# Kernel tuning notes

Hardware: AMD Instinct MI355X
Metric: run time of the kernel (lower is better)

## Reference

```python
import jax, jax.numpy as jnp
import numpy as np

EPS = 1e-15
MAX_TANH_ARG = 1.0 - 1e-5


def log_map_zero(x, c):
    sqrt_c = c ** 0.5
    n = jnp.clip(jnp.linalg.norm(x, axis=-1, keepdims=True), EPS, None)
    return jnp.arctanh(jnp.clip(sqrt_c * n, None, MAX_TANH_ARG)) * x / (sqrt_c * n)


def exp_map_zero(v, c):
    sqrt_c = c ** 0.5
    n = jnp.clip(jnp.linalg.norm(v, axis=-1, keepdims=True), EPS, None)
    return jnp.tanh(sqrt_c * n) * v / (sqrt_c * n)


def mobius_add(x, y, c):
    # ((1+2c<x,y>+c|y|^2) x + (1-c|x|^2) y) / (1+2c<x,y>+c^2|x|^2|y|^2)
    x2 = jnp.sum(x * x, axis=-1, keepdims=True)
    y2 = jnp.sum(y * y, axis=-1, keepdims=True)
    xy = jnp.sum(x * y, axis=-1, keepdims=True)
    num = (1.0 + 2.0 * c * xy + c * y2) * x + (1.0 - c * x2) * y
    den = 1.0 + 2.0 * c * xy + (c ** 2) * x2 * y2
    return num / jnp.clip(den, EPS, None)


def setup_inputs() -> dict:
    E, R, D, B = 100000, 500, 128, 512
    k = jax.random.split(jax.random.key(0), 7)
    entity_embedding = jax.random.normal(k[0], (E, D), dtype=jnp.float32) * 0.05
    rel_embedding = jax.random.normal(k[1], (R, D), dtype=jnp.float32) * 0.05
    s = jax.random.randint(k[2], (B,), 0, E)
    r = jax.random.randint(k[3], (B,), 0, R)
    o = jax.random.randint(k[4], (B,), 0, E)
    triplets = jnp.stack([s, r, o], axis=1).astype(jnp.int64)
    rel_diag = jax.random.uniform(k[5], (R, D), dtype=jnp.float32, minval=-1.0, maxval=1.0)
    rel_trans = jax.random.uniform(k[6], (R, D), dtype=jnp.float32, minval=-0.001, maxval=0.001)
    entity_bias = jnp.zeros((E,), dtype=jnp.float32)
    return {
        'entity_embedding': entity_embedding,
        'rel_embedding': rel_embedding,
        'triplets': triplets,
        'rel_diag': rel_diag,
        'rel_trans': rel_trans,
        'entity_bias': entity_bias,
    }


def _scores(entity_embedding, triplets, rel_diag, rel_trans, entity_bias, c=0.01):
    s_idx = triplets[:, 0]
    r_idx = triplets[:, 1]
    s_emb = entity_embedding[s_idx]                     # (B, D)
    rot = rel_diag[r_idx]                               # (B, D)
    # dropout p=0.0 -> identity
    rot_s = exp_map_zero(rot * log_map_zero(s_emb, c), c)
    t_r = exp_map_zero(rel_trans[r_idx], c)
    query = mobius_add(rot_s, t_r, c)                   # (B, D)

    # |(-q) (+)_c e|^2 in closed form from norms + one GEMM of dot products,
    # avoiding the O(B*E*D) expanded diff tensor of the original loop.
    q2 = jnp.sum(query * query, axis=-1)                # (B,)
    e2 = jnp.sum(entity_embedding * entity_embedding, axis=-1)  # (E,)
    dot = jnp.einsum('bd,ed->be', query, entity_embedding)      # (B, E)
    A = 1.0 - 2.0 * c * dot + c * e2[None, :]
    Bq = (1.0 - c * q2)[:, None]
    den = 1.0 - 2.0 * c * dot + (c ** 2) * q2[:, None] * e2[None, :]
    den = jnp.clip(den, EPS, None)
    num2 = A * A * q2[:, None] + Bq * Bq * e2[None, :] - 2.0 * A * Bq * dot
    dist_sq = num2 / (den * den)                        # (B, E)

    scores = -dist_sq + entity_bias[None, :] + entity_bias[s_idx][:, None]
    return scores


def reference(entity_embedding, rel_embedding, triplets, rel_diag, rel_trans, entity_bias):
    del rel_embedding  # kept for interface parity, unused in the original forward
    return _scores(entity_embedding, triplets, rel_diag, rel_trans, entity_bias, c=0.01)
```

## Files before the change

### kernel.cpp

```cpp
#include <hip/hip_runtime.h>
#include <hip/hip_bf16.h>
#include <math.h>

typedef short short8 __attribute__((ext_vector_type(8)));
typedef float f32x4  __attribute__((ext_vector_type(4)));

#define C_CURV 0.01f
#define SQRT_C 0.1f
#define EPSF   1e-15f
#define MAX_TANH 0.99999f

__device__ __forceinline__ unsigned short f32_to_bf16(float x) {
    unsigned u = __builtin_bit_cast(unsigned, x);
    u += 0x7FFFu + ((u >> 16) & 1u);
    return (unsigned short)(u >> 16);
}

__device__ __forceinline__ float wave_reduce_sum(float v) {
    #pragma unroll
    for (int off = 32; off > 0; off >>= 1)
        v += __shfl_xor(v, off, 64);
    return v;
}

__global__ __launch_bounds__(64)
void build_queries(const float* __restrict__ ent,
                   const int*   __restrict__ trip,
                   const float* __restrict__ rel_diag,
                   const float* __restrict__ rel_trans,
                   const float* __restrict__ ent_bias,
                   unsigned short* __restrict__ qh,
                   float* __restrict__ q2_out,
                   float* __restrict__ bs_out)
{
    const int b = blockIdx.x;
    const int d = threadIdx.x;
    const int s = trip[3 * b + 0];
    const int r = trip[3 * b + 1];

    const float* srow = ent + (size_t)s * 128;
    float x0 = srow[d], x1 = srow[d + 64];

    float n1 = fmaxf(sqrtf(wave_reduce_sum(x0 * x0 + x1 * x1)), EPSF);
    float a1 = atanhf(fminf(SQRT_C * n1, MAX_TANH)) / (SQRT_C * n1);
    float u0 = a1 * x0, u1 = a1 * x1;

    const float* rrow = rel_diag + (size_t)r * 128;
    float v0 = rrow[d] * u0, v1 = rrow[d + 64] * u1;
    float n2 = fmaxf(sqrtf(wave_reduce_sum(v0 * v0 + v1 * v1)), EPSF);
    float s2 = tanhf(SQRT_C * n2) / (SQRT_C * n2);
    float rs0 = s2 * v0, rs1 = s2 * v1;

    const float* trow = rel_trans + (size_t)r * 128;
    float t0 = trow[d], t1 = trow[d + 64];
    float n3 = fmaxf(sqrtf(wave_reduce_sum(t0 * t0 + t1 * t1)), EPSF);
    float s3 = tanhf(SQRT_C * n3) / (SQRT_C * n3);
    float tr0 = s3 * t0, tr1 = s3 * t1;

    float x2 = wave_reduce_sum(rs0 * rs0 + rs1 * rs1);
    float y2 = wave_reduce_sum(tr0 * tr0 + tr1 * tr1);
    float xy = wave_reduce_sum(rs0 * tr0 + rs1 * tr1);
    float cA = 1.f + 2.f * C_CURV * xy + C_CURV * y2;
    float cB = 1.f - C_CURV * x2;
    float den = 1.f + 2.f * C_CURV * xy + C_CURV * C_CURV * x2 * y2;
    den = fmaxf(den, EPSF);
    float inv = 1.f / den;
    float q0 = (cA * rs0 + cB * tr0) * inv;
    float q1 = (cA * rs1 + cB * tr1) * inv;

    float q2 = wave_reduce_sum(q0 * q0 + q1 * q1);

    qh[(size_t)b * 128 + d]      = f32_to_bf16(q0);
    qh[(size_t)b * 128 + d + 64] = f32_to_bf16(q1);
    if (d == 0) { q2_out[b] = q2; bs_out[b] = ent_bias[s]; }
}

__global__ __launch_bounds__(256, 3)
void gemm_score(const float* __restrict__ ent,
                const float* __restrict__ ent_bias,
                const unsigned short* __restrict__ qh,
                const float* __restrict__ q2a,
                const float* __restrict__ bsa,
                float* __restrict__ out,
                int E, int B)
{
    __shared__ char  EH[64 * 256];
    __shared__ float E2L[64];

    const int t = threadIdx.x;
    const int lane = t & 63, wid = t >> 6;
    const int l15 = lane & 15, lk = lane >> 4;
    const int r_ = t >> 2, h_ = t & 3;
    const int swzr = (r_ & 7) << 4;
    const int rswz = (l15 & 7) << 4;
    const float c = C_CURV;
    const int nbm = (B + 127) >> 7;
    const int tile = blockIdx.x;
    const int tb = tile * 64;

    {
        int g = tb + r_; if (g > E - 1) g = E - 1;
        const float4* src = (const float4*)(ent + (size_t)g * 128 + h_ * 32);
        float ss = 0.f;
        #pragma unroll
        for (int j = 0; j < 4; ++j) {
            float4 v0 = src[2 * j], v1 = src[2 * j + 1];
            short8 hi8;
            hi8[0] = (short)f32_to_bf16(v0.x); ss = fmaf(v0.x, v0.x, ss);
            hi8[1] = (short)f32_to_bf16(v0.y); ss = fmaf(v0.y, v0.y, ss);
            hi8[2] = (short)f32_to_bf16(v0.z); ss = fmaf(v0.z, v0.z, ss);
            hi8[3] = (short)f32_to_bf16(v0.w); ss = fmaf(v0.w, v0.w, ss);
            hi8[4] = (short)f32_to_bf16(v1.x); ss = fmaf(v1.x, v1.x, ss);
            hi8[5] = (short)f32_to_bf16(v1.y); ss = fmaf(v1.y, v1.y, ss);
            hi8[6] = (short)f32_to_bf16(v1.z); ss = fmaf(v1.z, v1.z, ss);
            hi8[7] = (short)f32_to_bf16(v1.w); ss = fmaf(v1.w, v1.w, ss);
            *(short8*)(EH + r_ * 256 + ((h_ * 64 + j * 16) ^ swzr)) = hi8;
        }
        ss += __shfl_xor(ss, 1, 64);
        ss += __shfl_xor(ss, 2, 64);
        if (h_ == 0) E2L[r_] = ss;
    }
    __syncthreads();

    float e2r[4], a02r[4], a0m2r[4], c2er[4], ber[4];
    unsigned cofs[4];
    bool cvr[4];
    #pragma unroll
    for (int n = 0; n < 4; ++n) {
        int col = tb + n * 16 + l15;
        cvr[n] = (col < E);
        int cc_ = cvr[n] ? col : (E - 1);
        float e2 = E2L[n * 16 + l15];
        float a0 = fmaf(c, e2, 1.f);
        e2r[n]   = e2;
        a02r[n]  = a0 * a0;
        a0m2r[n] = -2.f * a0;
        c2er[n]  = c * c * e2;
        ber[n]   = ent_bias[cc_];
        cofs[n]  = (unsigned)(tb + n * 16 + l15);
    }

    #pragma unroll 1
    for (int bm = 0; bm < nbm; ++bm) {
        const int bmb = bm << 7;

        short8 AH[2][4];
        #pragma unroll
        for (int m = 0; m < 2; ++m) {
            int ar = bmb + wid * 32 + m * 16 + l15;
            if (ar > B - 1) ar = B - 1;
            const char* ph = (const char*)qh + (size_t)ar * 256 + lk * 16;
            #pragma unroll
            for (int kk = 0; kk < 4; ++kk)
                AH[m][kk] = *(const short8*)(ph + kk * 64);
        }
        float q2r[8], b02r[8], Qrr[8], bsr[8];
        unsigned rowE[8];
        bool rvr[8];
        #pragma unroll
        for (int m = 0; m < 2; ++m)
        #pragma unroll
        for (int r = 0; r < 4; ++r) {
            const int i = m * 4 + r;
            int row = bmb + wid * 32 + m * 16 + lk * 4 + r;
            rvr[i] = (row < B);
            int rc = rvr[i] ? row : (B - 1);
            float q2 = q2a[rc];
            float b0 = fmaf(-c, q2, 1.f);
            q2r[i]  = q2;
            b02r[i] = b0 * b0;
            Qrr[i]  = fmaf(2.f * c, q2, b0);
            bsr[i]  = bsa[rc];
            rowE[i] = (unsigned)rc * (unsigned)E;
        }

        f32x4 acc[2][4];
        #pragma unroll
        for (int m = 0; m < 2; ++m)
            #pragma unroll
            for (int n = 0; n < 4; ++n)
                acc[m][n] = (f32x4){0.f, 0.f, 0.f, 0.f};

        #pragma unroll
        for (int kk = 0; kk < 4; ++kk) {
            short8 BH[4];
            const int ko = (kk * 64 + lk * 16) ^ rswz;
            #pragma unroll
            for (int n = 0; n < 4; ++n)
                BH[n] = *(const short8*)(EH + (n * 16 + l15) * 256 + ko);
            #pragma unroll
            for (int m = 0; m < 2; ++m)
                #pragma unroll
                for (int n = 0; n < 4; ++n)
                    acc[m][n] = __builtin_amdgcn_mfma_f32_16x16x32_bf16(AH[m][kk], BH[n], acc[m][n], 0, 0, 0);
        }

        #pragma unroll
        for (int m = 0; m < 2; ++m) {
            #pragma unroll
            for (int r = 0; r < 4; ++r) {
                const int i = m * 4 + r;
                const float q2 = q2r[i], b02 = b02r[i], Qr_ = Qrr[i], bs = bsr[i];
                #pragma unroll
                for (int n = 0; n < 4; ++n) {
                    const float d = acc[m][n][r];
                    float e0   = fmaf(c2er[n], q2, 1.f);
                    float den  = fmaf(-2.f * c, d, e0);
                    float inv  = __builtin_amdgcn_rcpf(den);
                    float P    = fmaf(a02r[n], q2, b02 * e2r[n]);
                    float Q    = a0m2r[n] * Qr_;
                    float num2 = fmaf(d, fmaf(4.f * c, d, Q), P);
                    float ni   = num2 * inv;
                    float sc   = fmaf(-ni, inv, ber[n] + bs);
                    if (cvr[n] && rvr[i])
                        out[rowE[i] + cofs[n]] = sc;
                }
            }
        }
    }
}

extern "C" void kernel_launch(void* const* d_in, const int* in_sizes, int n_in,
                              void* d_out, int out_size, void* d_ws, size_t ws_size,
                              hipStream_t stream) {
    const float* ent       = (const float*)d_in[0];
    const int*   trip      = (const int*)d_in[2];
    const float* rel_diag  = (const float*)d_in[3];
    const float* rel_trans = (const float*)d_in[4];
    const float* ent_bias  = (const float*)d_in[5];

    const int D = 128;
    const int E = in_sizes[0] / D;
    const int B = in_sizes[2] / 3;

    unsigned char* ws = (unsigned char*)d_ws;
    unsigned short* qh = (unsigned short*)ws;
    float* q2w = (float*)(ws + 131072);
    float* bsw = (float*)(ws + 131072 + 2048);

    build_queries<<<B, 64, 0, stream>>>(ent, trip, rel_diag, rel_trans, ent_bias,
                                        qh, q2w, bsw);

    const int ntiles = (E + 63) / 64;
    gemm_score<<<ntiles, 256, 0, stream>>>(ent, ent_bias, qh, q2w, bsw,
                                           (float*)d_out, E, B);
}
```

Baseline: 70.81 us.

## Shrink per-wave M tile and move column constants to LDS for occupancy

Each wave now processes 16 query rows per iteration instead of 32, so the B loop runs twice as many iterations with half the accumulators. The per-column constants (e2 terms, entity bias) are no longer kept in registers; e2 and bias are staged in LDS and recomputed each iteration. Launch bounds are raised from 3 to 4 blocks per CU to exploit the lower register pressure. The trade-off is more loop iterations, fewer MFMAs sharing each LDS B-fragment load, and extra ALU work in the epilogue in exchange for higher occupancy to hide the store-bound output writes.

```diff
diff --git a/kernel.cpp b/kernel.cpp
--- a/kernel.cpp
+++ b/kernel.cpp
@@ -75,7 +75,7 @@
     if (d == 0) { q2_out[b] = q2; bs_out[b] = ent_bias[s]; }
 }
 
-__global__ __launch_bounds__(256, 3)
+__global__ __launch_bounds__(256, 4)
 void gemm_score(const float* __restrict__ ent,
                 const float* __restrict__ ent_bias,
                 const unsigned short* __restrict__ qh,
@@ -85,7 +85,7 @@
                 int E, int B)
 {
     __shared__ char  EH[64 * 256];
-    __shared__ float E2L[64];
+    __shared__ float E2L[64], EBL[64];
 
     const int t = threadIdx.x;
     const int lane = t & 63, wid = t >> 6;
@@ -94,7 +94,7 @@
     const int swzr = (r_ & 7) << 4;
     const int rswz = (l15 & 7) << 4;
     const float c = C_CURV;
-    const int nbm = (B + 127) >> 7;
+    const int nbm = (B + 63) >> 6;
     const int tile = blockIdx.x;
     const int tb = tile * 64;
 
@@ -119,102 +119,81 @@
         ss += __shfl_xor(ss, 1, 64);
         ss += __shfl_xor(ss, 2, 64);
         if (h_ == 0) E2L[r_] = ss;
+        if (t < 64) { int gc = tb + t; if (gc > E - 1) gc = E - 1; EBL[t] = ent_bias[gc]; }
     }
     __syncthreads();
 
-    float e2r[4], a02r[4], a0m2r[4], c2er[4], ber[4];
-    unsigned cofs[4];
     bool cvr[4];
     #pragma unroll
-    for (int n = 0; n < 4; ++n) {
-        int col = tb + n * 16 + l15;
-        cvr[n] = (col < E);
-        int cc_ = cvr[n] ? col : (E - 1);
-        float e2 = E2L[n * 16 + l15];
-        float a0 = fmaf(c, e2, 1.f);
-        e2r[n]   = e2;
-        a02r[n]  = a0 * a0;
-        a0m2r[n] = -2.f * a0;
-        c2er[n]  = c * c * e2;
-        ber[n]   = ent_bias[cc_];
-        cofs[n]  = (unsigned)(tb + n * 16 + l15);
-    }
+    for (int n = 0; n < 4; ++n) cvr[n] = (tb + n * 16 + l15 < E);
 
     #pragma unroll 1
     for (int bm = 0; bm < nbm; ++bm) {
-        const int bmb = bm << 7;
-
-        short8 AH[2][4];
-        #pragma unroll
-        for (int m = 0; m < 2; ++m) {
-            int ar = bmb + wid * 32 + m * 16 + l15;
+        const int bmb = bm << 6;
+
+        short8 AH[4];
+        {
+            int ar = bmb + wid * 16 + l15;
             if (ar > B - 1) ar = B - 1;
             const char* ph = (const char*)qh + (size_t)ar * 256 + lk * 16;
             #pragma unroll
             for (int kk = 0; kk < 4; ++kk)
-                AH[m][kk] = *(const short8*)(ph + kk * 64);
-        }
-        float q2r[8], b02r[8], Qrr[8], bsr[8];
-        unsigned rowE[8];
-        bool rvr[8];
-        #pragma unroll
-        for (int m = 0; m < 2; ++m)
+                AH[kk] = *(const short8*)(ph + kk * 64);
+        }
+        float q2r[4], bsr[4];
         #pragma unroll
         for (int r = 0; r < 4; ++r) {
-            const int i = m * 4 + r;
-            int row = bmb + wid * 32 + m * 16 + lk * 4 + r;
-            rvr[i] = (row < B);
-            int rc = rvr[i] ? row : (B - 1);
-            float q2 = q2a[rc];
-            float b0 = fmaf(-c, q2, 1.f);
-            q2r[i]  = q2;
-            b02r[i] = b0 * b0;
-            Qrr[i]  = fmaf(2.f * c, q2, b0);
-            bsr[i]  = bsa[rc];
-            rowE[i] = (unsigned)rc * (unsigned)E;
-        }
-
-        f32x4 acc[2][4];
-        #pragma unroll
-        for (int m = 0; m < 2; ++m)
-            #pragma unroll
-            for (int n = 0; n < 4; ++n)
-                acc[m][n] = (f32x4){0.f, 0.f, 0.f, 0.f};
+            int row = bmb + wid * 16 + lk * 4 + r;
+            int rc = row < B ? row : (B - 1);
+            q2r[r] = q2a[rc];
+            bsr[r] = bsa[rc];
+        }
+
+        f32x4 acc[4];
+        #pragma unroll
+        for (int n = 0; n < 4; ++n) acc[n] = (f32x4){0.f, 0.f, 0.f, 0.f};
 
         #pragma unroll
         for (int kk = 0; kk < 4; ++kk) {
-            short8 BH[4];
             const int ko = (kk * 64 + lk * 16) ^ rswz;
             #pragma unroll
-            for (int n = 0; n < 4; ++n)
-                BH[n] = *(const short8*)(EH + (n * 16 + l15) * 256 + ko);
+            for (int n = 0; n < 4; ++n) {
+                short8 BH = *(const short8*)(EH + (n * 16 + l15) * 256 + ko);
+                acc[n] = __builtin_amdgcn_mfma_f32_16x16x32_bf16(AH[kk], BH, acc[n], 0, 0, 0);
+            }
+        }
+
+        float e2q[4], beq[4];
+        #pragma unroll
+        for (int n = 0; n < 4; ++n) {
+            e2q[n] = E2L[n * 16 + l15];
+            beq[n] = EBL[n * 16 + l15];
+        }
+
+        #pragma unroll
+        for (int r = 0; r < 4; ++r) {
+            const int row = bmb + wid * 16 + lk * 4 + r;
+            const float q2 = q2r[r];
+            const float b0 = fmaf(-c, q2, 1.f);
+            const float b02 = b0 * b0;
+            const float Qr_ = fmaf(2.f * c, q2, b0);
+            const float c2q2 = c * c * q2;
+            const unsigned base = (unsigned)row * (unsigned)E;
+            const bool rv = (row < B);
             #pragma unroll
-            for (int m = 0; m < 2; ++m)
-                #pragma unroll
-                for (int n = 0; n < 4; ++n)
-                    acc[m][n] = __builtin_amdgcn_mfma_f32_16x16x32_bf16(AH[m][kk], BH[n], acc[m][n], 0, 0, 0);
-        }
-
-        #pragma unroll
-        for (int m = 0; m < 2; ++m) {
-            #pragma unroll
-            for (int r = 0; r < 4; ++r) {
-                const int i = m * 4 + r;
-                const float q2 = q2r[i], b02 = b02r[i], Qr_ = Qrr[i], bs = bsr[i];
-                #pragma unroll
-                for (int n = 0; n < 4; ++n) {
-                    const float d = acc[m][n][r];
-                    float e0   = fmaf(c2er[n], q2, 1.f);
-                    float den  = fmaf(-2.f * c, d, e0);
-                    float inv  = __builtin_amdgcn_rcpf(den);
-                    float P    = fmaf(a02r[n], q2, b02 * e2r[n]);
-                    float Q    = a0m2r[n] * Qr_;
-                    float num2 = fmaf(d, fmaf(4.f * c, d, Q), P);
-                    float ni   = num2 * inv;
-                    float sc   = fmaf(-ni, inv, ber[n] + bs);
-                    if (cvr[n] && rvr[i])
-                        out[rowE[i] + cofs[n]] = sc;
-                }
+            for (int n = 0; n < 4; ++n) {
+                const float d  = acc[n][r];
+                const float e2 = e2q[n];
+                const float a0 = fmaf(c, e2, 1.f);
+                float den  = fmaf(-2.f * c, d, fmaf(c2q2, e2, 1.f));
+                float inv  = __builtin_amdgcn_rcpf(den);
+                float P    = fmaf(a0 * a0, q2, b02 * e2);
+                float Qp   = (-2.f * a0) * Qr_;
+                float num2 = fmaf(d, fmaf(4.f * c, d, Qp), P);
+                float ni   = num2 * inv;
+                float sc   = fmaf(-ni, inv, beq[n] + bsr[r]);
+                if (rv && cvr[n])
+                    out[base + (unsigned)(tb + n * 16 + l15)] = sc;
             }
         }
     }
```

Result: faster. 66.41 us (-6.2%).
